# Performance work log

Hardware: AMD Instinct MI355X
Metric: run time of the kernel (lower is better)

The kernel has to match this reference:

```python
import jax, jax.numpy as jnp
import numpy as np

HIDDEN = 32
N_STEPS = 64  # fixed-step RK4 replaces adaptive Dopri5 (same MLP-eval structure)
STD = 0.1     # init_params: Linear weights ~ N(0, 0.1), biases = 0


def _mlp(w1, b1, w2, b2, w3, b3, y):
    # NODE.forward: fc1 -> relu -> fc2 -> relu -> fc3 (t is unused in the source)
    h = jax.nn.relu(y @ w1 + b1)
    h = jax.nn.relu(h @ w2 + b2)
    return h @ w3 + b3


def setup_inputs() -> dict:
    key = jax.random.key(0)
    ks = jax.random.split(key, 8)
    B, D = 131072, 3
    x = jax.random.normal(ks[0], (B, D), dtype=jnp.float32)
    # eval times in (0.1, 1.0], sorted like a posterior-sample schedule
    samples = jnp.sort(
        jax.random.uniform(ks[1], (8, 1), jnp.float32, 0.1, 1.0), axis=0)
    w1 = (STD * jax.random.normal(ks[2], (D, HIDDEN))).astype(jnp.float32)
    b1 = jnp.zeros((HIDDEN,), jnp.float32)
    w2 = (STD * jax.random.normal(ks[3], (HIDDEN, HIDDEN))).astype(jnp.float32)
    b2 = jnp.zeros((HIDDEN,), jnp.float32)
    w3 = (STD * jax.random.normal(ks[4], (HIDDEN, D))).astype(jnp.float32)
    b3 = jnp.zeros((D,), jnp.float32)
    w_out = (STD * jax.random.normal(ks[5], (D, 1))).astype(jnp.float32)
    b_out = jnp.zeros((1,), jnp.float32)
    return {"x": x, "samples": samples, "w1": w1, "b1": b1, "w2": w2,
            "b2": b2, "w3": w3, "b3": b3, "w_out": w_out, "b_out": b_out}


def reference(x, samples, w1, b1, w2, b2, w3, b3, w_out, b_out):
    t_eval = samples[:, 0]                     # (S,)
    max_T = jnp.max(t_eval)
    dt = max_T / N_STEPS

    def step(y, _):
        k1 = _mlp(w1, b1, w2, b2, w3, b3, y)
        k2 = _mlp(w1, b1, w2, b2, w3, b3, y + 0.5 * dt * k1)
        k3 = _mlp(w1, b1, w2, b2, w3, b3, y + 0.5 * dt * k2)
        k4 = _mlp(w1, b1, w2, b2, w3, b3, y + dt * k3)
        y_new = y + (dt / 6.0) * (k1 + 2.0 * k2 + 2.0 * k3 + k4)
        return y_new, y_new

    # traj[i] is the state at time (i+1)*dt; shape (N_STEPS, B, 3)
    _, traj = jax.lax.scan(jax.checkpoint(step), x, jnp.arange(N_STEPS))

    # gather states at the grid step nearest each eval time
    idx = jnp.clip(jnp.round(t_eval / dt).astype(jnp.int32) - 1, 0, N_STEPS - 1)
    y_eval = traj[idx]                         # (S, B, 3)

    # fc_layers readout -> act_vec (S, B, 1)
    return y_eval @ w_out + b_out
```

## Files before the change

### kernel.cpp

```cpp
#include <hip/hip_runtime.h>

#define NSTEPS 64

typedef __attribute__((ext_vector_type(16))) float float16_;
typedef __attribute__((ext_vector_type(2))) __fp16 half2_;
typedef __attribute__((ext_vector_type(8))) __fp16 half8_;

__device__ __forceinline__ half2_ relu_pk_f16(float a, float b) {
    half2_ h = __builtin_amdgcn_cvt_pkrtz(a, b);
    return __builtin_elementwise_max(h, (half2_)(__fp16)0);
}

__global__ __launch_bounds__(256, 4)
void ode_rk4_mfma(const float* __restrict__ x,
                  const float* __restrict__ samples,
                  const float* __restrict__ w1, const float* __restrict__ b1,
                  const float* __restrict__ w2, const float* __restrict__ b2,
                  const float* __restrict__ w3, const float* __restrict__ b3,
                  const float* __restrict__ w_out, const float* __restrict__ b_out,
                  float* __restrict__ out, int B)
{
    const int lane  = threadIdx.x & 63;
    const int w     = threadIdx.x >> 6;
    const int col32 = lane & 31;
    const int half  = lane >> 5;

    const int rowBase = (blockIdx.x * 4 + w) * 32;
    const int row = rowBase + col32;

    auto pi = [](int m) -> int {
        int bb = (m >> 2) & 3;
        return m + ((bb == 1) ? 4 : (bb == 2) ? -4 : 0);
    };

    const float maxT = samples[7];
    const float dt   = maxT / 64.0f;
    const float dt2  = 0.5f * dt;
    const float dt6  = dt / 6.0f;

    union { half2_ h2[4]; half8_ h8; } A1h, A1f;
    {
        int pm = pi(col32);
        if (half == 0) {
            float w0 = w1[0 * 32 + pm], w1v = w1[1 * 32 + pm], w2v = w1[2 * 32 + pm];
            A1h.h2[0] = (half2_){(__fp16)w0, (__fp16)w1v};
            A1h.h2[1] = (half2_){(__fp16)w2v, (__fp16)b1[pm]};
            A1h.h2[2] = (half2_){(__fp16)(dt2 * w0), (__fp16)(dt2 * w1v)};
            A1h.h2[3] = (half2_){(__fp16)(dt2 * w2v), (__fp16)0.0f};
            A1f.h2[0] = A1h.h2[0];
            A1f.h2[1] = A1h.h2[1];
            A1f.h2[2] = (half2_){(__fp16)(dt * w0), (__fp16)(dt * w1v)};
            A1f.h2[3] = (half2_){(__fp16)(dt * w2v), (__fp16)0.0f};
        } else {
#pragma unroll
            for (int pp = 0; pp < 4; ++pp) {
                A1h.h2[pp] = (half2_)(__fp16)0.0f;
                A1f.h2[pp] = (half2_)(__fp16)0.0f;
            }
        }
    }

    union { half2_ h2[4]; half8_ h8; } W2T1, W2T2;
#pragma unroll
    for (int pp = 0; pp < 4; ++pp) {
        int i1 = half * 8 + 2 * pp;
        W2T1.h2[pp] = (half2_){(__fp16)w2[i1 * 32 + col32], (__fp16)w2[(i1 + 1) * 32 + col32]};
        W2T2.h2[pp] = (half2_){(__fp16)w2[(i1 + 16) * 32 + col32], (__fp16)w2[(i1 + 17) * 32 + col32]};
    }
    float16_ Cb;
#pragma unroll
    for (int r = 0; r < 16; ++r)
        Cb[r] = b2[(r & 3) + 8 * (r >> 2) + 4 * half];

    union { half2_ h2[4]; half8_ h8; } A31, A32;
    {
        const bool live = (col32 < 8) && ((col32 & 3) < 3);
        const int  d    = col32 & 3;
#pragma unroll
        for (int pp = 0; pp < 4; ++pp) {
            int j0 = 2 * pp;
            int nu0 = 4 * half + (j0 & 3) + 8 * (j0 >> 2);
            if (live) {
                A31.h2[pp] = (half2_){(__fp16)w3[nu0 * 3 + d], (__fp16)w3[(nu0 + 1) * 3 + d]};
                A32.h2[pp] = (half2_){(__fp16)w3[(nu0 + 16) * 3 + d], (__fp16)w3[(nu0 + 17) * 3 + d]};
            } else {
                A31.h2[pp] = (half2_)(__fp16)0.0f;
                A32.h2[pp] = (half2_)(__fp16)0.0f;
            }
        }
    }

    float16_ Zc;
#pragma unroll
    for (int r = 0; r < 16; ++r) Zc[r] = 0.0f;

    int sidx[8];
    unsigned long long smask = 0ull;
#pragma unroll
    for (int j = 0; j < 8; ++j) {
        int id = (int)rintf(samples[j] / dt) - 1;
        id = id < 0 ? 0 : (id > NSTEPS - 1 ? NSTEPS - 1 : id);
        id = __builtin_amdgcn_readfirstlane(id);
        sidx[j] = id;
        smask |= 1ull << id;
    }
    const float wo0 = w_out[0], wo1 = w_out[1], wo2 = w_out[2];
    const float bo  = b_out[0];
    const float b30 = b3[0], b31 = b3[1], b32 = b3[2];

    float y0 = x[(size_t)row * 3 + 0];
    float y1 = x[(size_t)row * 3 + 1];
    float y2 = x[(size_t)row * 3 + 2];

    const half2_ zh = (half2_)(__fp16)0.0f;

#pragma unroll 1
    for (int s = 0; s < NSTEPS; ++s) {
        float acc0 = 0.f, acc1 = 0.f, acc2 = 0.f;

        half2_ yp01 = __builtin_amdgcn_cvt_pkrtz(y0, y1);
        half2_ yp2o = __builtin_amdgcn_cvt_pkrtz(y2, 1.0f);

        float k0 = 0.f, k1 = 0.f, k2 = 0.f;

#pragma unroll
        for (int st = 0; st < 4; ++st) {
            half2_ kp01 = (st == 0) ? zh : __builtin_amdgcn_cvt_pkrtz(k0, k1);
            half2_ kp2o = (st == 0) ? zh : __builtin_amdgcn_cvt_pkrtz(k2, 0.0f);
            union { half2_ h2[4]; half8_ h8; } BL1;
            BL1.h2[0] = yp01; BL1.h2[1] = yp2o;
            BL1.h2[2] = kp01; BL1.h2[3] = kp2o;

            float16_ D1 = (st == 3)
                ? __builtin_amdgcn_mfma_f32_32x32x16_f16(A1f.h8, BL1.h8, Zc, 0, 0, 0)
                : __builtin_amdgcn_mfma_f32_32x32x16_f16(A1h.h8, BL1.h8, Zc, 0, 0, 0);

            union { half2_ h2[4]; half8_ h8; } B1, B2;
#pragma unroll
            for (int pp = 0; pp < 4; ++pp) {
                B1.h2[pp] = relu_pk_f16(D1[2 * pp], D1[2 * pp + 1]);
                B2.h2[pp] = relu_pk_f16(D1[8 + 2 * pp], D1[8 + 2 * pp + 1]);
            }

            float16_ D2 = __builtin_amdgcn_mfma_f32_32x32x16_f16(W2T1.h8, B1.h8,
                          __builtin_amdgcn_mfma_f32_32x32x16_f16(W2T2.h8, B2.h8, Cb, 0, 0, 0), 0, 0, 0);

            union { half2_ h2[4]; half8_ h8; } H1, H2;
#pragma unroll
            for (int pp = 0; pp < 4; ++pp) {
                H1.h2[pp] = relu_pk_f16(D2[2 * pp], D2[2 * pp + 1]);
                H2.h2[pp] = relu_pk_f16(D2[8 + 2 * pp], D2[8 + 2 * pp + 1]);
            }

            float16_ D3 = __builtin_amdgcn_mfma_f32_32x32x16_f16(A32.h8, H2.h8,
                          __builtin_amdgcn_mfma_f32_32x32x16_f16(A31.h8, H1.h8, Zc, 0, 0, 0), 0, 0, 0);

            k0 = D3[0] + b30;
            k1 = D3[1] + b31;
            k2 = D3[2] + b32;

            const float ca = (st == 1 || st == 2) ? 2.0f : 1.0f;
            acc0 = fmaf(ca, k0, acc0); acc1 = fmaf(ca, k1, acc1); acc2 = fmaf(ca, k2, acc2);
        }
        y0 = fmaf(dt6, acc0, y0); y1 = fmaf(dt6, acc1, y1); y2 = fmaf(dt6, acc2, y2);

        if ((smask >> s) & 1ull) {
            if (half == 0) {
#pragma unroll
                for (int j = 0; j < 8; ++j) {
                    if (sidx[j] == s) {
                        out[(size_t)j * B + row] = fmaf(y2, wo2, fmaf(y1, wo1, fmaf(y0, wo0, bo)));
                    }
                }
            }
        }
    }
}

extern "C" void kernel_launch(void* const* d_in, const int* in_sizes, int n_in,
                              void* d_out, int out_size, void* d_ws, size_t ws_size,
                              hipStream_t stream) {
    const float* x       = (const float*)d_in[0];
    const float* samples = (const float*)d_in[1];
    const float* w1      = (const float*)d_in[2];
    const float* b1      = (const float*)d_in[3];
    const float* w2      = (const float*)d_in[4];
    const float* b2      = (const float*)d_in[5];
    const float* w3      = (const float*)d_in[6];
    const float* b3      = (const float*)d_in[7];
    const float* w_out   = (const float*)d_in[8];
    const float* b_out   = (const float*)d_in[9];
    float* out = (float*)d_out;

    const int B = in_sizes[0] / 3;
    const int rowsPerBlock = 128;
    const int grid = (B + rowsPerBlock - 1) / rowsPerBlock;
    ode_rk4_mfma<<<grid, 256, 0, stream>>>(
        x, samples, w1, b1, w2, b2, w3, b3, w_out, b_out, out, B);
}
```

Measured before the change: 199.6 us.

## Switch MLP MFMAs to 16x16x32 tiles with 16 rows per wave

Replaces the 32x32x16 f16 MFMA chain, where each wave handles 32 batch rows, with 16x16x32 MFMAs that handle 16 rows per wave. Hidden-unit permutations and weight fragments are reorganised to fit the new tile shapes, and the fc3 bias is folded into the MFMA accumulator. The launch now uses 64 rows per block with an occupancy hint of 6. The aim is to shorten each wave's dependent MFMA latency chain and put more waves in flight to hide it. In exchange, the per-row scalar RK4 work runs on a quarter of the lanes instead of half, which costs more VALU issue per row.

```diff
diff --git a/kernel.cpp b/kernel.cpp
--- a/kernel.cpp
+++ b/kernel.cpp
@@ -2,16 +2,16 @@
 
 #define NSTEPS 64
 
-typedef __attribute__((ext_vector_type(16))) float float16_;
-typedef __attribute__((ext_vector_type(2))) __fp16 half2_;
-typedef __attribute__((ext_vector_type(8))) __fp16 half8_;
+typedef __attribute__((ext_vector_type(4)))  float  float4_;
+typedef __attribute__((ext_vector_type(2)))  __fp16 half2_;
+typedef __attribute__((ext_vector_type(8)))  __fp16 half8_;
 
 __device__ __forceinline__ half2_ relu_pk_f16(float a, float b) {
     half2_ h = __builtin_amdgcn_cvt_pkrtz(a, b);
     return __builtin_elementwise_max(h, (half2_)(__fp16)0);
 }
 
-__global__ __launch_bounds__(256, 4)
+__global__ __launch_bounds__(256, 6)
 void ode_rk4_mfma(const float* __restrict__ x,
                   const float* __restrict__ samples,
                   const float* __restrict__ w1, const float* __restrict__ b1,
@@ -22,15 +22,15 @@
 {
     const int lane  = threadIdx.x & 63;
     const int w     = threadIdx.x >> 6;
-    const int col32 = lane & 31;
-    const int half  = lane >> 5;
-
-    const int rowBase = (blockIdx.x * 4 + w) * 32;
-    const int row = rowBase + col32;
-
-    auto pi = [](int m) -> int {
-        int bb = (m >> 2) & 3;
-        return m + ((bb == 1) ? 4 : (bb == 2) ? -4 : 0);
+    const int col16 = lane & 15;
+    const int quad  = lane >> 4;
+
+    const int rowBase = (blockIdx.x * 4 + w) * 16;
+    const int row = rowBase + col16;
+
+    auto sig = [](int p) -> int {
+        int q = (p & 15) >> 2, r = p & 3;
+        return q * 8 + r + ((p < 16) ? 0 : 4);
     };
 
     const float maxT = samples[7];
@@ -38,61 +38,66 @@
     const float dt2  = 0.5f * dt;
     const float dt6  = dt / 6.0f;
 
-    union { half2_ h2[4]; half8_ h8; } A1h, A1f;
+    union F { half2_ h2[4]; half8_ h8; };
+    F A1h[2], A1f[2];
+#pragma unroll
+    for (int H = 0; H < 2; ++H) {
+        if (quad == 0) {
+            int u = sig(16 * H + col16);
+            float v0 = w1[0 * 32 + u], v1 = w1[1 * 32 + u], v2 = w1[2 * 32 + u];
+            float bb = b1[u];
+            A1h[H].h2[0] = (half2_){(__fp16)v0, (__fp16)v1};
+            A1h[H].h2[1] = (half2_){(__fp16)v2, (__fp16)bb};
+            A1h[H].h2[2] = (half2_){(__fp16)(dt2 * v0), (__fp16)(dt2 * v1)};
+            A1h[H].h2[3] = (half2_){(__fp16)(dt2 * v2), (__fp16)0.0f};
+            A1f[H].h2[0] = A1h[H].h2[0];
+            A1f[H].h2[1] = A1h[H].h2[1];
+            A1f[H].h2[2] = (half2_){(__fp16)(dt * v0), (__fp16)(dt * v1)};
+            A1f[H].h2[3] = (half2_){(__fp16)(dt * v2), (__fp16)0.0f};
+        } else {
+#pragma unroll
+            for (int pp = 0; pp < 4; ++pp) {
+                A1h[H].h2[pp] = (half2_)(__fp16)0.0f;
+                A1f[H].h2[pp] = (half2_)(__fp16)0.0f;
+            }
+        }
+    }
+
+    F A2[2];
+    float4_ Cb[2];
+#pragma unroll
+    for (int H = 0; H < 2; ++H) {
+        int u = sig(16 * H + col16);
+#pragma unroll
+        for (int pp = 0; pp < 4; ++pp) {
+            int kk = quad * 8 + 2 * pp;
+            A2[H].h2[pp] = (half2_){(__fp16)w2[kk * 32 + u], (__fp16)w2[(kk + 1) * 32 + u]};
+        }
+#pragma unroll
+        for (int r = 0; r < 4; ++r)
+            Cb[H][r] = b2[sig(16 * H + quad * 4 + r)];
+    }
+
+    F A3;
     {
-        int pm = pi(col32);
-        if (half == 0) {
-            float w0 = w1[0 * 32 + pm], w1v = w1[1 * 32 + pm], w2v = w1[2 * 32 + pm];
-            A1h.h2[0] = (half2_){(__fp16)w0, (__fp16)w1v};
-            A1h.h2[1] = (half2_){(__fp16)w2v, (__fp16)b1[pm]};
-            A1h.h2[2] = (half2_){(__fp16)(dt2 * w0), (__fp16)(dt2 * w1v)};
-            A1h.h2[3] = (half2_){(__fp16)(dt2 * w2v), (__fp16)0.0f};
-            A1f.h2[0] = A1h.h2[0];
-            A1f.h2[1] = A1h.h2[1];
-            A1f.h2[2] = (half2_){(__fp16)(dt * w0), (__fp16)(dt * w1v)};
-            A1f.h2[3] = (half2_){(__fp16)(dt * w2v), (__fp16)0.0f};
-        } else {
-#pragma unroll
-            for (int pp = 0; pp < 4; ++pp) {
-                A1h.h2[pp] = (half2_)(__fp16)0.0f;
-                A1f.h2[pp] = (half2_)(__fp16)0.0f;
-            }
-        }
-    }
-
-    union { half2_ h2[4]; half8_ h8; } W2T1, W2T2;
-#pragma unroll
-    for (int pp = 0; pp < 4; ++pp) {
-        int i1 = half * 8 + 2 * pp;
-        W2T1.h2[pp] = (half2_){(__fp16)w2[i1 * 32 + col32], (__fp16)w2[(i1 + 1) * 32 + col32]};
-        W2T2.h2[pp] = (half2_){(__fp16)w2[(i1 + 16) * 32 + col32], (__fp16)w2[(i1 + 17) * 32 + col32]};
-    }
-    float16_ Cb;
-#pragma unroll
-    for (int r = 0; r < 16; ++r)
-        Cb[r] = b2[(r & 3) + 8 * (r >> 2) + 4 * half];
-
-    union { half2_ h2[4]; half8_ h8; } A31, A32;
-    {
-        const bool live = (col32 < 8) && ((col32 & 3) < 3);
-        const int  d    = col32 & 3;
+        const int  d    = col16 & 3;
+        const bool live = d < 3;
 #pragma unroll
         for (int pp = 0; pp < 4; ++pp) {
-            int j0 = 2 * pp;
-            int nu0 = 4 * half + (j0 & 3) + 8 * (j0 >> 2);
-            if (live) {
-                A31.h2[pp] = (half2_){(__fp16)w3[nu0 * 3 + d], (__fp16)w3[(nu0 + 1) * 3 + d]};
-                A32.h2[pp] = (half2_){(__fp16)w3[(nu0 + 16) * 3 + d], (__fp16)w3[(nu0 + 17) * 3 + d]};
-            } else {
-                A31.h2[pp] = (half2_)(__fp16)0.0f;
-                A32.h2[pp] = (half2_)(__fp16)0.0f;
-            }
-        }
-    }
-
-    float16_ Zc;
-#pragma unroll
-    for (int r = 0; r < 16; ++r) Zc[r] = 0.0f;
+            int kk = quad * 8 + 2 * pp;
+            A3.h2[pp] = live
+                ? (half2_){(__fp16)w3[kk * 3 + d], (__fp16)w3[(kk + 1) * 3 + d]}
+                : (half2_)(__fp16)0.0f;
+        }
+    }
+    float4_ C3;
+#pragma unroll
+    for (int r = 0; r < 4; ++r)
+        C3[r] = (r < 3) ? b3[r] : 0.0f;
+
+    float4_ Zc;
+#pragma unroll
+    for (int r = 0; r < 4; ++r) Zc[r] = 0.0f;
 
     int sidx[8];
     unsigned long long smask = 0ull;
@@ -106,7 +111,6 @@
     }
     const float wo0 = w_out[0], wo1 = w_out[1], wo2 = w_out[2];
     const float bo  = b_out[0];
-    const float b30 = b3[0], b31 = b3[1], b32 = b3[2];
 
     float y0 = x[(size_t)row * 3 + 0];
     float y1 = x[(size_t)row * 3 + 1];
@@ -127,37 +131,39 @@
         for (int st = 0; st < 4; ++st) {
             half2_ kp01 = (st == 0) ? zh : __builtin_amdgcn_cvt_pkrtz(k0, k1);
             half2_ kp2o = (st == 0) ? zh : __builtin_amdgcn_cvt_pkrtz(k2, 0.0f);
-            union { half2_ h2[4]; half8_ h8; } BL1;
+            F BL1;
             BL1.h2[0] = yp01; BL1.h2[1] = yp2o;
             BL1.h2[2] = kp01; BL1.h2[3] = kp2o;
 
-            float16_ D1 = (st == 3)
-                ? __builtin_amdgcn_mfma_f32_32x32x16_f16(A1f.h8, BL1.h8, Zc, 0, 0, 0)
-                : __builtin_amdgcn_mfma_f32_32x32x16_f16(A1h.h8, BL1.h8, Zc, 0, 0, 0);
-
-            union { half2_ h2[4]; half8_ h8; } B1, B2;
-#pragma unroll
-            for (int pp = 0; pp < 4; ++pp) {
-                B1.h2[pp] = relu_pk_f16(D1[2 * pp], D1[2 * pp + 1]);
-                B2.h2[pp] = relu_pk_f16(D1[8 + 2 * pp], D1[8 + 2 * pp + 1]);
+            float4_ D1_0, D1_1;
+            if (st == 3) {
+                D1_0 = __builtin_amdgcn_mfma_f32_16x16x32_f16(A1f[0].h8, BL1.h8, Zc, 0, 0, 0);
+                D1_1 = __builtin_amdgcn_mfma_f32_16x16x32_f16(A1f[1].h8, BL1.h8, Zc, 0, 0, 0);
+            } else {
+                D1_0 = __builtin_amdgcn_mfma_f32_16x16x32_f16(A1h[0].h8, BL1.h8, Zc, 0, 0, 0);
+                D1_1 = __builtin_amdgcn_mfma_f32_16x16x32_f16(A1h[1].h8, BL1.h8, Zc, 0, 0, 0);
             }
 
-            float16_ D2 = __builtin_amdgcn_mfma_f32_32x32x16_f16(W2T1.h8, B1.h8,
-                          __builtin_amdgcn_mfma_f32_32x32x16_f16(W2T2.h8, B2.h8, Cb, 0, 0, 0), 0, 0, 0);
-
-            union { half2_ h2[4]; half8_ h8; } H1, H2;
-#pragma unroll
-            for (int pp = 0; pp < 4; ++pp) {
-                H1.h2[pp] = relu_pk_f16(D2[2 * pp], D2[2 * pp + 1]);
-                H2.h2[pp] = relu_pk_f16(D2[8 + 2 * pp], D2[8 + 2 * pp + 1]);
-            }
-
-            float16_ D3 = __builtin_amdgcn_mfma_f32_32x32x16_f16(A32.h8, H2.h8,
-                          __builtin_amdgcn_mfma_f32_32x32x16_f16(A31.h8, H1.h8, Zc, 0, 0, 0), 0, 0, 0);
-
-            k0 = D3[0] + b30;
-            k1 = D3[1] + b31;
-            k2 = D3[2] + b32;
+            F P;
+            P.h2[0] = relu_pk_f16(D1_0[0], D1_0[1]);
+            P.h2[1] = relu_pk_f16(D1_0[2], D1_0[3]);
+            P.h2[2] = relu_pk_f16(D1_1[0], D1_1[1]);
+            P.h2[3] = relu_pk_f16(D1_1[2], D1_1[3]);
+
+            float4_ D2_0 = __builtin_amdgcn_mfma_f32_16x16x32_f16(A2[0].h8, P.h8, Cb[0], 0, 0, 0);
+            float4_ D2_1 = __builtin_amdgcn_mfma_f32_16x16x32_f16(A2[1].h8, P.h8, Cb[1], 0, 0, 0);
+
+            F Q;
+            Q.h2[0] = relu_pk_f16(D2_0[0], D2_0[1]);
+            Q.h2[1] = relu_pk_f16(D2_0[2], D2_0[3]);
+            Q.h2[2] = relu_pk_f16(D2_1[0], D2_1[1]);
+            Q.h2[3] = relu_pk_f16(D2_1[2], D2_1[3]);
+
+            float4_ D3 = __builtin_amdgcn_mfma_f32_16x16x32_f16(A3.h8, Q.h8, C3, 0, 0, 0);
+
+            k0 = D3[0];
+            k1 = D3[1];
+            k2 = D3[2];
 
             const float ca = (st == 1 || st == 2) ? 2.0f : 1.0f;
             acc0 = fmaf(ca, k0, acc0); acc1 = fmaf(ca, k1, acc1); acc2 = fmaf(ca, k2, acc2);
@@ -165,7 +171,7 @@
         y0 = fmaf(dt6, acc0, y0); y1 = fmaf(dt6, acc1, y1); y2 = fmaf(dt6, acc2, y2);
 
         if ((smask >> s) & 1ull) {
-            if (half == 0) {
+            if (quad == 0) {
 #pragma unroll
                 for (int j = 0; j < 8; ++j) {
                     if (sidx[j] == s) {
@@ -193,7 +199,7 @@
     float* out = (float*)d_out;
 
     const int B = in_sizes[0] / 3;
-    const int rowsPerBlock = 128;
+    const int rowsPerBlock = 64;
     const int grid = (B + rowsPerBlock - 1) / rowsPerBlock;
     ode_rk4_mfma<<<grid, 256, 0, stream>>>(
         x, samples, w1, b1, w2, b2, w3, b3, w_out, b_out, out, B);
```

After: 215.2 us. +7.8%, slower.
